# Optimization experiments

Hardware: AMD Instinct MI355X
Metric: run time of the kernel (lower is better)

The kernel has to match this reference:

```python
import jax, jax.numpy as jnp
import numpy as np

HIDDEN = 768
BATCH = 128


def setup_inputs() -> dict:
    key = jax.random.key(0)
    k_in, k_op = jax.random.split(key)
    inputs = jax.random.normal(k_in, (BATCH, HIDDEN, HIDDEN), dtype=jnp.float32)
    # nn.init.uniform_(operator, 0, 1)
    operator = jax.random.uniform(k_op, (HIDDEN, HIDDEN), dtype=jnp.float32)
    return {"inputs": inputs, "operator": operator}


def reference(inputs, operator):
    # Original: diag(operator @ inputs @ operator^T) then softmax over dim axis.
    # diag_i = sum_{j,k} operator[i,j] * inputs[b,j,k] * operator[i,k]
    # Compute first GEMM, then fuse the second matmul's diagonal as a dot-reduction.
    mm = jnp.einsum('ij,bjk->bik', operator, inputs)      # [b, d, d]
    diag = jnp.einsum('bik,ik->bi', mm, operator)          # [b, d]
    return jax.nn.softmax(diag, axis=1)
```

## Files before the change

### kernel.cpp

```cpp
#include <hip/hip_runtime.h>

#define HID 768
#define NB  128

typedef _Float16 half8   __attribute__((ext_vector_type(8)));
typedef __fp16   fp16x2  __attribute__((ext_vector_type(2)));
typedef float    float4_t __attribute__((ext_vector_type(4)));

#define OP_TILES (48 * 24)
#define OP_PLANE ((size_t)OP_TILES * 64 * 8)

__global__ __launch_bounds__(256)
void split_op(const float* __restrict__ OP, _Float16* __restrict__ ws)
{
    const int g    = blockIdx.x * 256 + threadIdx.x;
    const int tile = g >> 6, lane = g & 63;
    const int it16 = tile / 24, ks = tile % 24;
    const int i = it16 * 16 + (lane & 15);
    const int k = ks * 32 + (lane >> 4) * 8;
    const float4_t a = *(const float4_t*)(OP + (size_t)i * HID + k);
    const float4_t b = *(const float4_t*)(OP + (size_t)i * HID + k + 4);
    half8 h, l;
#pragma unroll
    for (int e = 0; e < 4; ++e) {
        _Float16 h0 = (_Float16)a[e]; h[e]     = h0; l[e]     = (_Float16)(a[e] - (float)h0);
        _Float16 h1 = (_Float16)b[e]; h[e + 4] = h1; l[e + 4] = (_Float16)(b[e] - (float)h1);
    }
    *(half8*)(ws + (size_t)(tile * 64 + lane) * 8) = h;
    *(half8*)(ws + OP_PLANE + (size_t)(tile * 64 + lane) * 8) = l;
}

__device__ __forceinline__ void convert8(const float4_t a, const float4_t b,
                                         half8& h, half8& l)
{
    fp16x2 h01 = __builtin_amdgcn_cvt_pkrtz(a[0], a[1]);
    fp16x2 h23 = __builtin_amdgcn_cvt_pkrtz(a[2], a[3]);
    fp16x2 h45 = __builtin_amdgcn_cvt_pkrtz(b[0], b[1]);
    fp16x2 h67 = __builtin_amdgcn_cvt_pkrtz(b[2], b[3]);
    fp16x2 l01 = __builtin_amdgcn_cvt_pkrtz(a[0] - (float)h01[0], a[1] - (float)h01[1]);
    fp16x2 l23 = __builtin_amdgcn_cvt_pkrtz(a[2] - (float)h23[0], a[3] - (float)h23[1]);
    fp16x2 l45 = __builtin_amdgcn_cvt_pkrtz(b[0] - (float)h45[0], b[1] - (float)h45[1]);
    fp16x2 l67 = __builtin_amdgcn_cvt_pkrtz(b[2] - (float)h67[0], b[3] - (float)h67[1]);
    h = (half8){(_Float16)h01[0], (_Float16)h01[1], (_Float16)h23[0], (_Float16)h23[1],
                (_Float16)h45[0], (_Float16)h45[1], (_Float16)h67[0], (_Float16)h67[1]};
    l = (half8){(_Float16)l01[0], (_Float16)l01[1], (_Float16)l23[0], (_Float16)l23[1],
                (_Float16)l45[0], (_Float16)l45[1], (_Float16)l67[0], (_Float16)l67[1]};
}

__global__ __launch_bounds__(256, 3)
void diag_quad_kernel(const float* __restrict__ X, const float* __restrict__ OP,
                      const _Float16* __restrict__ opws, float* __restrict__ out)
{
    __shared__ __align__(16) _Float16 Ah[4096];
    __shared__ __align__(16) _Float16 Al[4096];
    __shared__ float Dred[2][128];

    const int idx  = blockIdx.x;
    const int xcd  = idx & 7, slot = idx >> 3;
    const int b    = xcd * 16 + slot / 6;
    const int it   = slot % 6;
    const int i0   = it * 128;
    const float* Xb = X + (size_t)b * HID * HID;

    const int tid  = threadIdx.x;
    const int lane = tid & 63;
    const int wave = tid >> 6;
    const int wj   = wave & 1;
    const int wi   = wave >> 1;
    const int m16  = lane & 15;
    const int kg   = lane >> 4;

    const int row0 = tid >> 2;
    const int kgs  = tid & 3;
    const int m16s = row0 & 15;
    const int swz  = (m16s ^ (kgs << 1)) * 8;
    const int lds0 = (row0 >> 4) * 512 + kgs * 128 + swz;
    const int lds1 = ((row0 + 64) >> 4) * 512 + kgs * 128 + swz;

    const int fragoff  = kg * 128 + (m16 ^ (kg << 1)) * 8;
    const int it16base = it * 8 + wi * 4;

    float p[4] = {0.f, 0.f, 0.f, 0.f};

    for (int jt = 0; jt < 6; ++jt) {
        const int j0 = jt * 128;
        float4_t acc[4][4];
#pragma unroll
        for (int a = 0; a < 4; ++a)
#pragma unroll
            for (int c = 0; c < 4; ++c) acc[a][c] = (float4_t){0.f, 0.f, 0.f, 0.f};

        for (int ks = 0; ks < 24; ++ks) {
            const int k0 = ks * 32;

            half8 bh[4], bl[4];
            const size_t obase = ((size_t)it16base * 24 + ks) * 512 + (size_t)lane * 8;
#pragma unroll
            for (int tj = 0; tj < 4; ++tj) {
                bh[tj] = *(const half8*)(opws + obase + (size_t)tj * 24 * 512);
                bl[tj] = *(const half8*)(opws + OP_PLANE + obase + (size_t)tj * 24 * 512);
            }

            const float* s0 = Xb + (size_t)(j0 + row0) * HID + k0 + kgs * 8;
            const float* s1 = Xb + (size_t)(j0 + row0 + 64) * HID + k0 + kgs * 8;
            const float4_t a0 = *(const float4_t*)(s0);
            const float4_t a1 = *(const float4_t*)(s0 + 4);
            const float4_t b0 = *(const float4_t*)(s1);
            const float4_t b1 = *(const float4_t*)(s1 + 4);
            half8 h0, l0v, h1, l1v;
            convert8(a0, a1, h0, l0v);
            convert8(b0, b1, h1, l1v);

            __syncthreads();
            *(half8*)&Ah[lds0] = h0;
            *(half8*)&Al[lds0] = l0v;
            *(half8*)&Ah[lds1] = h1;
            *(half8*)&Al[lds1] = l1v;
            __syncthreads();

#pragma unroll
            for (int ti = 0; ti < 4; ++ti) {
                const int off = (wj * 4 + ti) * 512 + fragoff;
                const half8 ah = *(const half8*)&Ah[off];
                const half8 al = *(const half8*)&Al[off];
#pragma unroll
                for (int tj = 0; tj < 4; ++tj) {
                    acc[ti][tj] = __builtin_amdgcn_mfma_f32_16x16x32_f16(ah, bh[tj], acc[ti][tj], 0, 0, 0);
                    acc[ti][tj] = __builtin_amdgcn_mfma_f32_16x16x32_f16(al, bh[tj], acc[ti][tj], 0, 0, 0);
                    acc[ti][tj] = __builtin_amdgcn_mfma_f32_16x16x32_f16(ah, bl[tj], acc[ti][tj], 0, 0, 0);
                }
            }
        }

#pragma unroll
        for (int tj = 0; tj < 4; ++tj) {
            const int i_abs = i0 + wi * 64 + tj * 16 + m16;
            float s = 0.f;
#pragma unroll
            for (int ti = 0; ti < 4; ++ti) {
                const int jb = j0 + wj * 64 + ti * 16 + kg * 4;
                const float4_t ov = *(const float4_t*)(OP + (size_t)i_abs * HID + jb);
#pragma unroll
                for (int r = 0; r < 4; ++r) s += acc[ti][tj][r] * ov[r];
            }
            p[tj] += s;
        }
    }

#pragma unroll
    for (int tj = 0; tj < 4; ++tj) {
        p[tj] += __shfl_xor(p[tj], 16);
        p[tj] += __shfl_xor(p[tj], 32);
    }
    if (kg == 0) {
#pragma unroll
        for (int tj = 0; tj < 4; ++tj)
            Dred[wj][wi * 64 + tj * 16 + m16] = p[tj];
    }
    __syncthreads();
    if (tid < 128)
        out[(size_t)b * HID + i0 + tid] = Dred[0][tid] + Dred[1][tid];
}

__global__ __launch_bounds__(768)
void softmax_rows(float* __restrict__ out)
{
    const int row = blockIdx.x;
    const int t = threadIdx.x;
    const int wave = t >> 6, lane = t & 63;
    __shared__ float redm[12];
    __shared__ float reds[12];

    float v = out[(size_t)row * HID + t];

    float m = v;
#pragma unroll
    for (int o = 32; o >= 1; o >>= 1) m = fmaxf(m, __shfl_xor(m, o));
    if (lane == 0) redm[wave] = m;
    __syncthreads();
    if (t == 0) {
        float mm = redm[0];
        for (int w = 1; w < 12; ++w) mm = fmaxf(mm, redm[w]);
        redm[0] = mm;
    }
    __syncthreads();
    m = redm[0];

    const float e = expf(v - m);
    float s = e;
#pragma unroll
    for (int o = 32; o >= 1; o >>= 1) s += __shfl_xor(s, o);
    if (lane == 0) reds[wave] = s;
    __syncthreads();
    if (t == 0) {
        float ss = 0.f;
        for (int w = 0; w < 12; ++w) ss += reds[w];
        reds[0] = ss;
    }
    __syncthreads();
    out[(size_t)row * HID + t] = e / reds[0];
}

extern "C" void kernel_launch(void* const* d_in, const int* in_sizes, int n_in,
                              void* d_out, int out_size, void* d_ws, size_t ws_size,
                              hipStream_t stream)
{
    const float* X  = (const float*)d_in[0];
    const float* OP = (const float*)d_in[1];
    float* out = (float*)d_out;
    _Float16* opws = (_Float16*)d_ws;

    hipLaunchKernelGGL(split_op, dim3(OP_TILES / 4), dim3(256), 0, stream, OP, opws);
    hipLaunchKernelGGL(diag_quad_kernel, dim3(NB * 6), dim3(256), 0, stream, X, OP, opws, out);
    hipLaunchKernelGGL(softmax_rows, dim3(NB), dim3(768), 0, stream, out);
}
```

Baseline: 632.2 us.

## Prefetch next X tile into registers during MFMA compute in flattened loop

```diff
diff --git a/kernel.cpp b/kernel.cpp
--- a/kernel.cpp
+++ b/kernel.cpp
@@ -82,69 +82,94 @@
 
     float p[4] = {0.f, 0.f, 0.f, 0.f};
 
-    for (int jt = 0; jt < 6; ++jt) {
+    {
+        const float* s0 = Xb + (size_t)row0 * HID + kgs * 8;
+        const float* s1 = Xb + (size_t)(row0 + 64) * HID + kgs * 8;
+        const float4_t a0 = *(const float4_t*)(s0);
+        const float4_t a1 = *(const float4_t*)(s0 + 4);
+        const float4_t b0 = *(const float4_t*)(s1);
+        const float4_t b1 = *(const float4_t*)(s1 + 4);
+        half8 h0, l0v, h1, l1v;
+        convert8(a0, a1, h0, l0v);
+        convert8(b0, b1, h1, l1v);
+        *(half8*)&Ah[lds0] = h0;
+        *(half8*)&Al[lds0] = l0v;
+        *(half8*)&Ah[lds1] = h1;
+        *(half8*)&Al[lds1] = l1v;
+        __syncthreads();
+    }
+
+    float4_t acc[4][4];
+    int jt = 0, ks = 0;
+    for (int t = 0; t < 144; ++t) {
         const int j0 = jt * 128;
-        float4_t acc[4][4];
-#pragma unroll
-        for (int a = 0; a < 4; ++a)
-#pragma unroll
-            for (int c = 0; c < 4; ++c) acc[a][c] = (float4_t){0.f, 0.f, 0.f, 0.f};
-
-        for (int ks = 0; ks < 24; ++ks) {
-            const int k0 = ks * 32;
-
-            half8 bh[4], bl[4];
-            const size_t obase = ((size_t)it16base * 24 + ks) * 512 + (size_t)lane * 8;
+
+        half8 bh[4], bl[4];
+        const size_t obase = ((size_t)it16base * 24 + ks) * 512 + (size_t)lane * 8;
+#pragma unroll
+        for (int tj = 0; tj < 4; ++tj) {
+            bh[tj] = *(const half8*)(opws + obase + (size_t)tj * 24 * 512);
+            bl[tj] = *(const half8*)(opws + OP_PLANE + obase + (size_t)tj * 24 * 512);
+        }
+
+        int kn = ks + 1, jn = jt;
+        if (kn == 24) { kn = 0; ++jn; }
+        const int jcl = (jn < 6) ? jn : 0;
+        const float* s0 = Xb + (size_t)(jcl * 128 + row0) * HID + kn * 32 + kgs * 8;
+        const float* s1 = s0 + (size_t)64 * HID;
+        const float4_t a0 = *(const float4_t*)(s0);
+        const float4_t a1 = *(const float4_t*)(s0 + 4);
+        const float4_t b0 = *(const float4_t*)(s1);
+        const float4_t b1 = *(const float4_t*)(s1 + 4);
+
+        if (ks == 0) {
+#pragma unroll
+            for (int a = 0; a < 4; ++a)
+#pragma unroll
+                for (int c = 0; c < 4; ++c) acc[a][c] = (float4_t){0.f, 0.f, 0.f, 0.f};
+        }
+
+#pragma unroll
+        for (int ti = 0; ti < 4; ++ti) {
+            const int off = (wj * 4 + ti) * 512 + fragoff;
+            const half8 ah = *(const half8*)&Ah[off];
+            const half8 al = *(const half8*)&Al[off];
 #pragma unroll
             for (int tj = 0; tj < 4; ++tj) {
-                bh[tj] = *(const half8*)(opws + obase + (size_t)tj * 24 * 512);
-                bl[tj] = *(const half8*)(opws + OP_PLANE + obase + (size_t)tj * 24 * 512);
+                acc[ti][tj] = __builtin_amdgcn_mfma_f32_16x16x32_f16(ah, bh[tj], acc[ti][tj], 0, 0, 0);
+                acc[ti][tj] = __builtin_amdgcn_mfma_f32_16x16x32_f16(al, bh[tj], acc[ti][tj], 0, 0, 0);
+                acc[ti][tj] = __builtin_amdgcn_mfma_f32_16x16x32_f16(ah, bl[tj], acc[ti][tj], 0, 0, 0);
             }
-
-            const float* s0 = Xb + (size_t)(j0 + row0) * HID + k0 + kgs * 8;
-            const float* s1 = Xb + (size_t)(j0 + row0 + 64) * HID + k0 + kgs * 8;
-            const float4_t a0 = *(const float4_t*)(s0);
-            const float4_t a1 = *(const float4_t*)(s0 + 4);
-            const float4_t b0 = *(const float4_t*)(s1);
-            const float4_t b1 = *(const float4_t*)(s1 + 4);
-            half8 h0, l0v, h1, l1v;
-            convert8(a0, a1, h0, l0v);
-            convert8(b0, b1, h1, l1v);
-
-            __syncthreads();
-            *(half8*)&Ah[lds0] = h0;
-            *(half8*)&Al[lds0] = l0v;
-            *(half8*)&Ah[lds1] = h1;
-            *(half8*)&Al[lds1] = l1v;
-            __syncthreads();
-
-#pragma unroll
-            for (int ti = 0; ti < 4; ++ti) {
-                const int off = (wj * 4 + ti) * 512 + fragoff;
-                const half8 ah = *(const half8*)&Ah[off];
-                const half8 al = *(const half8*)&Al[off];
-#pragma unroll
-                for (int tj = 0; tj < 4; ++tj) {
-                    acc[ti][tj] = __builtin_amdgcn_mfma_f32_16x16x32_f16(ah, bh[tj], acc[ti][tj], 0, 0, 0);
-                    acc[ti][tj] = __builtin_amdgcn_mfma_f32_16x16x32_f16(al, bh[tj], acc[ti][tj], 0, 0, 0);
-                    acc[ti][tj] = __builtin_amdgcn_mfma_f32_16x16x32_f16(ah, bl[tj], acc[ti][tj], 0, 0, 0);
+        }
+
+        if (ks == 23) {
+#pragma unroll
+            for (int tj = 0; tj < 4; ++tj) {
+                const int i_abs = i0 + wi * 64 + tj * 16 + m16;
+                float s = 0.f;
+#pragma unroll
+                for (int ti = 0; ti < 4; ++ti) {
+                    const int jb = j0 + wj * 64 + ti * 16 + kg * 4;
+                    const float4_t ov = *(const float4_t*)(OP + (size_t)i_abs * HID + jb);
+#pragma unroll
+                    for (int r = 0; r < 4; ++r) s += acc[ti][tj][r] * ov[r];
                 }
+                p[tj] += s;
             }
         }
 
-#pragma unroll
-        for (int tj = 0; tj < 4; ++tj) {
-            const int i_abs = i0 + wi * 64 + tj * 16 + m16;
-            float s = 0.f;
-#pragma unroll
-            for (int ti = 0; ti < 4; ++ti) {
-                const int jb = j0 + wj * 64 + ti * 16 + kg * 4;
-                const float4_t ov = *(const float4_t*)(OP + (size_t)i_abs * HID + jb);
-#pragma unroll
-                for (int r = 0; r < 4; ++r) s += acc[ti][tj][r] * ov[r];
-            }
-            p[tj] += s;
-        }
+        half8 h0, l0v, h1, l1v;
+        convert8(a0, a1, h0, l0v);
+        convert8(b0, b1, h1, l1v);
+
+        __syncthreads();
+        *(half8*)&Ah[lds0] = h0;
+        *(half8*)&Al[lds0] = l0v;
+        *(half8*)&Ah[lds1] = h1;
+        *(half8*)&Al[lds1] = l1v;
+        __syncthreads();
+
+        jt = jn; ks = kn;
     }
 
 #pragma unroll
```

After: 629.6 us. Within noise of the previous version (-0.4%).
